# Performance work log

Measured on AMD Instinct MI355X. Metric: run time of the kernel, lower is better.

Reference implementation:

```python
import jax, jax.numpy as jnp
import numpy as np

NUM_HEADS = 16

def setup_inputs() -> dict:
    key = jax.random.key(0)
    k1, k2, k3 = jax.random.split(key, 3)
    B, N, C = 4, 4096, 1024
    x = jax.random.normal(k1, (B, N, C), dtype=jnp.float32)
    y = jax.random.normal(k2, (B, N, C), dtype=jnp.float32)
    # nn.Linear(embed_dim, embed_dim): weight [C, C], bias [C]
    W_proj = jax.random.normal(k3, (C, C), dtype=jnp.float32) * (1.0 / np.sqrt(C))
    b_proj = jnp.zeros((C,), dtype=jnp.float32)
    return {"x": x, "y": y, "W_proj": W_proj, "b_proj": b_proj}

def reference(x, y, W_proj, b_proj):
    B, N, C = x.shape
    H = NUM_HEADS
    d = C // H
    # NOTE: no head transpose in the original -> scores are over the HEAD axis.
    q = x.reshape(B, N, H, d)
    k = y.reshape(B, N, H, d)
    v = y.reshape(B, N, H, d)
    # attn: [B, N, H, H], per-token head-to-head scores
    attn = jnp.einsum('bnhd,bngd->bnhg', q, k) / jnp.sqrt(jnp.asarray(d, x.dtype))
    attn = jax.nn.softmax(attn, axis=-1)
    # dropout(p=0.1) is identity in eval mode
    o = jnp.einsum('bnhg,bngd->bnhd', attn, v)          # [B, N, H, d]
    # x.transpose(1, 2).reshape(B, N, C) in torch:
    o = jnp.transpose(o, (0, 2, 1, 3)).reshape(B, N, C)
    out = o @ W_proj.T + b_proj
    return out
```

## Files before the change

kernel.cpp:

```cpp
#include <hip/hip_runtime.h>
#include <hip/hip_bf16.h>
#include <stdint.h>

typedef __attribute__((ext_vector_type(8))) short bf16x8;
typedef __attribute__((ext_vector_type(4))) short bf16x4;
typedef __attribute__((ext_vector_type(4))) float f32x4;
typedef __attribute__((ext_vector_type(4))) int   i32x4;

static __device__ __forceinline__ short f2bs(float f) {
  __hip_bfloat16 h = __float2bfloat16(f);
  return __builtin_bit_cast(short, h);
}

__device__ __forceinline__ void gload_lds16(const void* g, void* l) {
  auto* gp = reinterpret_cast<__attribute__((address_space(1))) uint32_t*>((uintptr_t)g);
  auto* lp = reinterpret_cast<__attribute__((address_space(3))) uint32_t*>((uintptr_t)l);
  __builtin_amdgcn_global_load_lds(gp, lp, 16, 0, 0);
}

__global__ __launch_bounds__(256) void attn_kernel(
    const float* __restrict__ x, const float* __restrict__ y,
    __hip_bfloat16* __restrict__ A)
{
  const int wid  = threadIdx.x >> 6;
  const int lane = threadIdx.x & 63;
  const int tok  = blockIdx.x * 4 + wid;
  const int b    = tok >> 12;
  const int n    = tok & 4095;

  const float* xr = x + (size_t)tok * 1024;
  const float* yr = y + (size_t)tok * 1024;

  const int c  = lane & 15;
  const int qq = lane >> 4;

  const int fbase = c * 64 + qq * 8;
  bf16x8 yf[2], xf[2];
  #pragma unroll
  for (int kk = 0; kk < 2; ++kk) {
    const float4 a0 = *(const float4*)(yr + fbase + kk * 32);
    const float4 a1 = *(const float4*)(yr + fbase + kk * 32 + 4);
    const float4 b0 = *(const float4*)(xr + fbase + kk * 32);
    const float4 b1 = *(const float4*)(xr + fbase + kk * 32 + 4);
    yf[kk] = bf16x8{f2bs(a0.x), f2bs(a0.y), f2bs(a0.z), f2bs(a0.w),
                    f2bs(a1.x), f2bs(a1.y), f2bs(a1.z), f2bs(a1.w)};
    xf[kk] = bf16x8{f2bs(b0.x), f2bs(b0.y), f2bs(b0.z), f2bs(b0.w),
                    f2bs(b1.x), f2bs(b1.y), f2bs(b1.z), f2bs(b1.w)};
  }

  f32x4 acc = {0.f, 0.f, 0.f, 0.f};
  acc = __builtin_amdgcn_mfma_f32_16x16x32_bf16(yf[0], xf[0], acc, 0, 0, 0);
  acc = __builtin_amdgcn_mfma_f32_16x16x32_bf16(yf[1], xf[1], acc, 0, 0, 0);

  float sc[4];
  #pragma unroll
  for (int r = 0; r < 4; ++r) sc[r] = acc[r] * 0.125f;
  float mx = fmaxf(fmaxf(sc[0], sc[1]), fmaxf(sc[2], sc[3]));
  mx = fmaxf(mx, __shfl_xor(mx, 16));
  mx = fmaxf(mx, __shfl_xor(mx, 32));
  float e[4];
  #pragma unroll
  for (int r = 0; r < 4; ++r) e[r] = __expf(sc[r] - mx);
  float sm = (e[0] + e[1]) + (e[2] + e[3]);
  sm += __shfl_xor(sm, 16);
  sm += __shfl_xor(sm, 32);
  const float inv = 1.0f / sm;
  float p[4];
  #pragma unroll
  for (int r = 0; r < 4; ++r) p[r] = e[r] * inv;

  f32x4 o[4];
  #pragma unroll
  for (int q = 0; q < 4; ++q) o[q] = f32x4{0.f, 0.f, 0.f, 0.f};

#if __has_builtin(__builtin_amdgcn_mfma_f32_16x16x16bf16_1k)
  const bf16x4 pa = {f2bs(p[0]), f2bs(p[1]), f2bs(p[2]), f2bs(p[3])};
  #pragma unroll
  for (int q = 0; q < 4; ++q) {
    bf16x4 bq;
    #pragma unroll
    for (int j = 0; j < 4; ++j)
      bq[j] = f2bs(yr[(qq * 4 + j) * 64 + q * 16 + c]);
    o[q] = __builtin_amdgcn_mfma_f32_16x16x16bf16_1k(pa, bq, o[q], 0, 0, 0);
  }
#else
  const int u0 = ((int)(unsigned short)f2bs(p[1]) << 16) | (unsigned short)f2bs(p[0]);
  const int u1 = ((int)(unsigned short)f2bs(p[3]) << 16) | (unsigned short)f2bs(p[2]);
  const int s0 = c + 32 * qq;
  int a0 = __shfl(u0, s0), a1 = __shfl(u1, s0);
  int a2 = __shfl(u0, s0 + 16), a3 = __shfl(u1, s0 + 16);
  const bool valid = (qq < 2);
  if (!valid) { a0 = 0; a1 = 0; a2 = 0; a3 = 0; }
  const bf16x8 a8 = __builtin_bit_cast(bf16x8, i32x4{a0, a1, a2, a3});
  #pragma unroll
  for (int q = 0; q < 4; ++q) {
    bf16x8 b8;
    #pragma unroll
    for (int j = 0; j < 8; ++j) {
      const int g = (qq * 8 + j) & 15;
      const float v = yr[g * 64 + q * 16 + c];
      b8[j] = valid ? f2bs(v) : (short)0;
    }
    o[q] = __builtin_amdgcn_mfma_f32_16x16x32_bf16(a8, b8, o[q], 0, 0, 0);
  }
#endif

  const size_t base = ((size_t)b * 4096 + (n >> 4)) * 1024 + ((n & 15) << 6) + c;
  #pragma unroll
  for (int q = 0; q < 4; ++q)
    #pragma unroll
    for (int r = 0; r < 4; ++r) {
      const int h = qq * 4 + r;
      A[base + (size_t)h * 262144 + q * 16] = __float2bfloat16(o[q][r]);
    }
}

__global__ __launch_bounds__(256) void wcvt_kernel(const float* __restrict__ w,
                                                   __hip_bfloat16* __restrict__ wb)
{
  const int i = (blockIdx.x * 256 + threadIdx.x) * 4;
  const float4 v = *(const float4*)(w + i);
  wb[i + 0] = __float2bfloat16(v.x);
  wb[i + 1] = __float2bfloat16(v.y);
  wb[i + 2] = __float2bfloat16(v.z);
  wb[i + 3] = __float2bfloat16(v.w);
}

#define BM 128
#define BN 128
#define BK 32

__global__ __launch_bounds__(256) void gemm_bt_bias(
    const __hip_bfloat16* __restrict__ A,
    const __hip_bfloat16* __restrict__ Bw,
    const float* __restrict__ bias,
    float* __restrict__ C)
{
  constexpr int Nn = 1024, K = 1024;
  __shared__ __hip_bfloat16 As[BM * BK];
  __shared__ __hip_bfloat16 Bs[BN * BK];

  const int tid  = threadIdx.x;
  const int lane = tid & 63;
  const int wid  = tid >> 6;
  const int wr   = wid >> 1, wc = wid & 1;

  const int bid = blockIdx.y * 8 + blockIdx.x;
  const int nb  = (bid & 7) * 128 + (bid >> 3);
  const int mBase = (nb >> 3) * BM;
  const int nBase = (nb & 7) * BN;

  const int srow = tid >> 2;
  const int scol = (tid & 3) * 8;
  const __hip_bfloat16* aSrc0 = A  + (size_t)(mBase + srow)      * K + scol;
  const __hip_bfloat16* aSrc1 = A  + (size_t)(mBase + 64 + srow) * K + scol;
  const __hip_bfloat16* bSrc0 = Bw + (size_t)(nBase + srow)      * K + scol;
  const __hip_bfloat16* bSrc1 = Bw + (size_t)(nBase + 64 + srow) * K + scol;
  char* aDst0 = (char*)As + tid * 16;
  char* aDst1 = (char*)As + 4096 + tid * 16;
  char* bDst0 = (char*)Bs + tid * 16;
  char* bDst1 = (char*)Bs + 4096 + tid * 16;

  f32x4 acc[4][4];
  const f32x4 fzero = {0.f, 0.f, 0.f, 0.f};
  #pragma unroll
  for (int m = 0; m < 4; ++m)
    #pragma unroll
    for (int n = 0; n < 4; ++n) acc[m][n] = fzero;

  const int fr = lane & 15;
  const int kb = (lane >> 4) * 8;

  for (int k0 = 0; k0 < K; k0 += BK) {
    gload_lds16(aSrc0 + k0, aDst0);
    gload_lds16(aSrc1 + k0, aDst1);
    gload_lds16(bSrc0 + k0, bDst0);
    gload_lds16(bSrc1 + k0, bDst1);
    __syncthreads();

    bf16x8 af[4], bfr[4];
    #pragma unroll
    for (int m = 0; m < 4; ++m)
      af[m] = *(const bf16x8*)&As[(wr * 64 + m * 16 + fr) * BK + kb];
    #pragma unroll
    for (int n = 0; n < 4; ++n)
      bfr[n] = *(const bf16x8*)&Bs[(wc * 64 + n * 16 + fr) * BK + kb];

    #pragma unroll
    for (int m = 0; m < 4; ++m)
      #pragma unroll
      for (int n = 0; n < 4; ++n)
        acc[m][n] = __builtin_amdgcn_mfma_f32_16x16x32_bf16(af[m], bfr[n], acc[m][n], 0, 0, 0);
    __syncthreads();
  }

  const int fq = lane >> 4;
  #pragma unroll
  for (int n = 0; n < 4; ++n) {
    const int col = nBase + wc * 64 + n * 16 + fr;
    const float bv = bias[col];
    #pragma unroll
    for (int m = 0; m < 4; ++m) {
      const int row0 = mBase + wr * 64 + m * 16 + fq * 4;
      #pragma unroll
      for (int r = 0; r < 4; ++r)
        C[(size_t)(row0 + r) * Nn + col] = acc[m][n][r] + bv;
    }
  }
}

extern "C" void kernel_launch(void* const* d_in, const int* in_sizes, int n_in,
                              void* d_out, int out_size, void* d_ws, size_t ws_size,
                              hipStream_t stream) {
  const float* x    = (const float*)d_in[0];
  const float* y    = (const float*)d_in[1];
  const float* W    = (const float*)d_in[2];
  const float* bias = (const float*)d_in[3];
  float* out = (float*)d_out;

  __hip_bfloat16* Abuf = (__hip_bfloat16*)d_ws;
  __hip_bfloat16* Wbuf = (__hip_bfloat16*)((char*)d_ws + (size_t)16384 * 1024 * 2);

  wcvt_kernel<<<1024, 256, 0, stream>>>(W, Wbuf);
  attn_kernel<<<4096, 256, 0, stream>>>(x, y, Abuf);
  gemm_bt_bias<<<dim3(8, 128), 256, 0, stream>>>(Abuf, Wbuf, bias, out);
}
```

Baseline: 89.40 us.

## Replace projection GEMM with 256x256 double-buffered, swizzled 8-wave kernel

Rewrites the output projection GEMM to use 256x256 tiles with BK=64, 512 threads (8 waves), and double-buffered LDS. Global-to-LDS loads for the next K tile are issued while MFMAs run on the current one, and an XOR swizzle on LDS columns avoids bank conflicts. Explicit barriers, waitcnt and setprio interleave the load and compute phases. The aim is more data reuse per tile and hidden memory latency, at the cost of higher register/LDS use and only 256 blocks.

```diff
diff --git a/kernel.cpp b/kernel.cpp
--- a/kernel.cpp
+++ b/kernel.cpp
@@ -126,72 +126,143 @@
   wb[i + 3] = __float2bfloat16(v.w);
 }
 
-#define BM 128
-#define BN 128
-#define BK 32
-
-__global__ __launch_bounds__(256) void gemm_bt_bias(
+#define NT 16
+
+#define FENCE asm volatile("" ::: "memory")
+#define BAR   __builtin_amdgcn_s_barrier()
+
+#define STAGE_A(toff, b) do {                                           \
+    gload_lds16(aSrc + (toff),          aDst + (b) * 32768);            \
+    gload_lds16(aSrc + (toff) + 131072, aDst + (b) * 32768 + 8192);     \
+    gload_lds16(aSrc + (toff) + 262144, aDst + (b) * 32768 + 16384);    \
+    gload_lds16(aSrc + (toff) + 393216, aDst + (b) * 32768 + 24576);    \
+  } while (0)
+
+#define STAGE_B(toff, b) do {                                           \
+    gload_lds16(bSrc + (toff),          bDst + (b) * 32768);            \
+    gload_lds16(bSrc + (toff) + 131072, bDst + (b) * 32768 + 8192);     \
+    gload_lds16(bSrc + (toff) + 262144, bDst + (b) * 32768 + 16384);    \
+    gload_lds16(bSrc + (toff) + 393216, bDst + (b) * 32768 + 24576);    \
+  } while (0)
+
+__global__ __launch_bounds__(512, 2) void gemm256(
     const __hip_bfloat16* __restrict__ A,
     const __hip_bfloat16* __restrict__ Bw,
     const float* __restrict__ bias,
     float* __restrict__ C)
 {
-  constexpr int Nn = 1024, K = 1024;
-  __shared__ __hip_bfloat16 As[BM * BK];
-  __shared__ __hip_bfloat16 Bs[BN * BK];
+  constexpr int K = 1024, Nn = 1024;
+  __shared__ char ldsA[2 * 32768];
+  __shared__ char ldsB[2 * 32768];
 
   const int tid  = threadIdx.x;
   const int lane = tid & 63;
   const int wid  = tid >> 6;
-  const int wr   = wid >> 1, wc = wid & 1;
-
-  const int bid = blockIdx.y * 8 + blockIdx.x;
-  const int nb  = (bid & 7) * 128 + (bid >> 3);
-  const int mBase = (nb >> 3) * BM;
-  const int nBase = (nb & 7) * BN;
-
-  const int srow = tid >> 2;
-  const int scol = (tid & 3) * 8;
-  const __hip_bfloat16* aSrc0 = A  + (size_t)(mBase + srow)      * K + scol;
-  const __hip_bfloat16* aSrc1 = A  + (size_t)(mBase + 64 + srow) * K + scol;
-  const __hip_bfloat16* bSrc0 = Bw + (size_t)(nBase + srow)      * K + scol;
-  const __hip_bfloat16* bSrc1 = Bw + (size_t)(nBase + 64 + srow) * K + scol;
-  char* aDst0 = (char*)As + tid * 16;
-  char* aDst1 = (char*)As + 4096 + tid * 16;
-  char* bDst0 = (char*)Bs + tid * 16;
-  char* bDst1 = (char*)Bs + 4096 + tid * 16;
-
-  f32x4 acc[4][4];
-  const f32x4 fzero = {0.f, 0.f, 0.f, 0.f};
-  #pragma unroll
-  for (int m = 0; m < 4; ++m)
-    #pragma unroll
-    for (int n = 0; n < 4; ++n) acc[m][n] = fzero;
+  const int wr   = wid >> 2;
+  const int wc   = wid & 3;
+
+  const int bid = blockIdx.x;
+  const int nb  = (bid & 7) * 32 + (bid >> 3);
+  const int mBase = (nb >> 2) * 256;
+  const int nBase = (nb & 3) * 256;
+
+  const int srow = tid >> 3;
+  const int pcb  = (tid & 7) << 4;
+  const int lcb  = pcb ^ ((srow & 7) << 4);
+  const char* aSrc = (const char*)A  + ((size_t)(mBase + srow) * K) * 2 + lcb;
+  const char* bSrc = (const char*)Bw + ((size_t)(nBase + srow) * K) * 2 + lcb;
+  char* aDst = ldsA + tid * 16;
+  char* bDst = ldsB + tid * 16;
 
   const int fr = lane & 15;
-  const int kb = (lane >> 4) * 8;
-
-  for (int k0 = 0; k0 < K; k0 += BK) {
-    gload_lds16(aSrc0 + k0, aDst0);
-    gload_lds16(aSrc1 + k0, aDst1);
-    gload_lds16(bSrc0 + k0, bDst0);
-    gload_lds16(bSrc1 + k0, bDst1);
-    __syncthreads();
-
-    bf16x8 af[4], bfr[4];
-    #pragma unroll
-    for (int m = 0; m < 4; ++m)
-      af[m] = *(const bf16x8*)&As[(wr * 64 + m * 16 + fr) * BK + kb];
-    #pragma unroll
-    for (int n = 0; n < 4; ++n)
-      bfr[n] = *(const bf16x8*)&Bs[(wc * 64 + n * 16 + fr) * BK + kb];
-
-    #pragma unroll
-    for (int m = 0; m < 4; ++m)
-      #pragma unroll
-      for (int n = 0; n < 4; ++n)
-        acc[m][n] = __builtin_amdgcn_mfma_f32_16x16x32_bf16(af[m], bfr[n], acc[m][n], 0, 0, 0);
-    __syncthreads();
+  const int kq = lane >> 4;
+  const int xr = (fr & 7) << 4;
+  const int ofk0 = ((kq << 4))      ^ xr;
+  const int ofk1 = (64 + (kq << 4)) ^ xr;
+  const char* aRow = ldsA + (wr * 128 + fr) * 128;
+  const char* bRow = ldsB + (wc * 64  + fr) * 128;
+
+  f32x4 acc[8][4];
+  #pragma unroll
+  for (int m = 0; m < 8; ++m)
+    #pragma unroll
+    for (int n = 0; n < 4; ++n) acc[m][n] = f32x4{0.f, 0.f, 0.f, 0.f};
+
+  STAGE_A(0, 0);
+  STAGE_B(0, 0);
+  asm volatile("s_waitcnt vmcnt(0)" ::: "memory");
+  BAR;
+
+  for (int t = 0; t < NT; ++t) {
+    const int cur  = t & 1;
+    const int nxt  = cur ^ 1;
+    const int toff = (t + 1) * 128;
+    const char* aR = aRow + cur * 32768;
+    const char* bR = bRow + cur * 32768;
+    bf16x8 Af[4], Bf[4];
+
+    if (t + 1 < NT) STAGE_A(toff, nxt);
+    #pragma unroll
+    for (int n = 0; n < 4; ++n) Bf[n] = *(const bf16x8*)(bR + n * 2048 + ofk0);
+    #pragma unroll
+    for (int m = 0; m < 4; ++m) Af[m] = *(const bf16x8*)(aR + m * 2048 + ofk0);
+    FENCE; BAR;
+    asm volatile("s_waitcnt lgkmcnt(0)" ::: "memory");
+    __builtin_amdgcn_sched_barrier(0);
+    __builtin_amdgcn_s_setprio(1);
+    #pragma unroll
+    for (int m = 0; m < 4; ++m)
+      #pragma unroll
+      for (int n = 0; n < 4; ++n)
+        acc[m][n] = __builtin_amdgcn_mfma_f32_16x16x32_bf16(Af[m], Bf[n], acc[m][n], 0, 0, 0);
+    __builtin_amdgcn_s_setprio(0);
+    FENCE; BAR;
+
+    if (t + 1 < NT) STAGE_B(toff, nxt);
+    #pragma unroll
+    for (int m = 0; m < 4; ++m) Af[m] = *(const bf16x8*)(aR + (4 + m) * 2048 + ofk0);
+    FENCE; BAR;
+    asm volatile("s_waitcnt lgkmcnt(0)" ::: "memory");
+    __builtin_amdgcn_sched_barrier(0);
+    __builtin_amdgcn_s_setprio(1);
+    #pragma unroll
+    for (int m = 0; m < 4; ++m)
+      #pragma unroll
+      for (int n = 0; n < 4; ++n)
+        acc[4 + m][n] = __builtin_amdgcn_mfma_f32_16x16x32_bf16(Af[m], Bf[n], acc[4 + m][n], 0, 0, 0);
+    __builtin_amdgcn_s_setprio(0);
+    FENCE; BAR;
+
+    #pragma unroll
+    for (int n = 0; n < 4; ++n) Bf[n] = *(const bf16x8*)(bR + n * 2048 + ofk1);
+    #pragma unroll
+    for (int m = 0; m < 4; ++m) Af[m] = *(const bf16x8*)(aR + m * 2048 + ofk1);
+    FENCE; BAR;
+    asm volatile("s_waitcnt lgkmcnt(0)" ::: "memory");
+    __builtin_amdgcn_sched_barrier(0);
+    __builtin_amdgcn_s_setprio(1);
+    #pragma unroll
+    for (int m = 0; m < 4; ++m)
+      #pragma unroll
+      for (int n = 0; n < 4; ++n)
+        acc[m][n] = __builtin_amdgcn_mfma_f32_16x16x32_bf16(Af[m], Bf[n], acc[m][n], 0, 0, 0);
+    __builtin_amdgcn_s_setprio(0);
+    FENCE; BAR;
+
+    #pragma unroll
+    for (int m = 0; m < 4; ++m) Af[m] = *(const bf16x8*)(aR + (4 + m) * 2048 + ofk1);
+    FENCE; BAR;
+    asm volatile("s_waitcnt lgkmcnt(0)" ::: "memory");
+    __builtin_amdgcn_sched_barrier(0);
+    __builtin_amdgcn_s_setprio(1);
+    #pragma unroll
+    for (int m = 0; m < 4; ++m)
+      #pragma unroll
+      for (int n = 0; n < 4; ++n)
+        acc[4 + m][n] = __builtin_amdgcn_mfma_f32_16x16x32_bf16(Af[m], Bf[n], acc[4 + m][n], 0, 0, 0);
+    __builtin_amdgcn_s_setprio(0);
+    if (t + 1 < NT) asm volatile("s_waitcnt vmcnt(0)" ::: "memory");
+    FENCE; BAR;
   }
 
   const int fq = lane >> 4;
@@ -200,8 +271,8 @@
     const int col = nBase + wc * 64 + n * 16 + fr;
     const float bv = bias[col];
     #pragma unroll
-    for (int m = 0; m < 4; ++m) {
-      const int row0 = mBase + wr * 64 + m * 16 + fq * 4;
+    for (int m = 0; m < 8; ++m) {
+      const int row0 = mBase + wr * 128 + m * 16 + fq * 4;
       #pragma unroll
       for (int r = 0; r < 4; ++r)
         C[(size_t)(row0 + r) * Nn + col] = acc[m][n][r] + bv;
@@ -223,5 +294,5 @@
 
   wcvt_kernel<<<1024, 256, 0, stream>>>(W, Wbuf);
   attn_kernel<<<4096, 256, 0, stream>>>(x, y, Abuf);
-  gemm_bt_bias<<<dim3(8, 128), 256, 0, stream>>>(Abuf, Wbuf, bias, out);
-}
+  gemm256<<<256, 512, 0, stream>>>(Abuf, Wbuf, bias, out);
+}
```

New measurement: 76.39 us. -14.6%, faster.

## Triple-buffer GEMM LDS loads with XOR swizzle and manual waitcnt pipeline

Applied to the files above, without the earlier changes.

Rewrites the projection GEMM so it keeps three LDS stages in flight. Global-to-LDS loads for tile t+2 are issued while tile t is computed, with explicit vmcnt waits and a single barrier per tile, replacing the two syncthreads per K step. LDS addresses are XOR-swizzled to cut bank conflicts on the fragment reads. MFMA issue priority is raised and occupancy is hinted to 3 blocks per CU. This adds hand-written waitcnt ordering that must stay correct, and it uses more LDS per block.

```diff
diff --git a/kernel.cpp b/kernel.cpp
--- a/kernel.cpp
+++ b/kernel.cpp
@@ -126,78 +126,102 @@
   wb[i + 3] = __float2bfloat16(v.w);
 }
 
-#define BM 128
-#define BN 128
-#define BK 32
-
-__global__ __launch_bounds__(256) void gemm_bt_bias(
+#define NT 32
+
+#define FENCE asm volatile("" ::: "memory")
+#define BAR   __builtin_amdgcn_s_barrier()
+#define LGKM0 asm volatile("s_waitcnt lgkmcnt(0)" ::: "memory")
+#define VM4   asm volatile("s_waitcnt vmcnt(4)" ::: "memory")
+#define VM0   asm volatile("s_waitcnt vmcnt(0)" ::: "memory")
+#define SB0   __builtin_amdgcn_sched_barrier(0)
+#define SP1   __builtin_amdgcn_s_setprio(1)
+#define SP0   __builtin_amdgcn_s_setprio(0)
+
+#define STAGE(toff, bo) do {                                        \
+    gload_lds16(aSrc + (toff),          aDst + (bo));               \
+    gload_lds16(aSrc + (toff) + 131072, aDst + (bo) + 4096);        \
+    gload_lds16(bSrc + (toff),          bDst + (bo));               \
+    gload_lds16(bSrc + (toff) + 131072, bDst + (bo) + 4096);        \
+  } while (0)
+
+__global__ __launch_bounds__(256, 3) void gemm128(
     const __hip_bfloat16* __restrict__ A,
     const __hip_bfloat16* __restrict__ Bw,
     const float* __restrict__ bias,
     float* __restrict__ C)
 {
-  constexpr int Nn = 1024, K = 1024;
-  __shared__ __hip_bfloat16 As[BM * BK];
-  __shared__ __hip_bfloat16 Bs[BN * BK];
+  constexpr int K = 1024, Nn = 1024;
+  __shared__ char ldsA[3 * 8192];
+  __shared__ char ldsB[3 * 8192];
 
   const int tid  = threadIdx.x;
   const int lane = tid & 63;
   const int wid  = tid >> 6;
-  const int wr   = wid >> 1, wc = wid & 1;
-
-  const int bid = blockIdx.y * 8 + blockIdx.x;
+  const int wr   = wid >> 1;
+  const int wcN  = wid & 1;
+
+  const int bid = blockIdx.x;
   const int nb  = (bid & 7) * 128 + (bid >> 3);
-  const int mBase = (nb >> 3) * BM;
-  const int nBase = (nb & 7) * BN;
+  const int mBase = (nb >> 3) * 128;
+  const int nBase = (nb & 7) * 128;
 
   const int srow = tid >> 2;
-  const int scol = (tid & 3) * 8;
-  const __hip_bfloat16* aSrc0 = A  + (size_t)(mBase + srow)      * K + scol;
-  const __hip_bfloat16* aSrc1 = A  + (size_t)(mBase + 64 + srow) * K + scol;
-  const __hip_bfloat16* bSrc0 = Bw + (size_t)(nBase + srow)      * K + scol;
-  const __hip_bfloat16* bSrc1 = Bw + (size_t)(nBase + 64 + srow) * K + scol;
-  char* aDst0 = (char*)As + tid * 16;
-  char* aDst1 = (char*)As + 4096 + tid * 16;
-  char* bDst0 = (char*)Bs + tid * 16;
-  char* bDst1 = (char*)Bs + 4096 + tid * 16;
+  const int lcb  = (((tid & 3) ^ ((tid >> 3) & 3)) << 4);
+  const char* aSrc = (const char*)A  + (size_t)(mBase + srow) * (K * 2) + lcb;
+  const char* bSrc = (const char*)Bw + (size_t)(nBase + srow) * (K * 2) + lcb;
+  char* aDst = ldsA + tid * 16;
+  char* bDst = ldsB + tid * 16;
+
+  const int fr = lane & 15;
+  const int kq = lane >> 4;
+  const int ofk  = ((kq ^ ((fr >> 1) & 3)) << 4);
+  const int aOff = (wr  * 64 + fr) * 64 + ofk;
+  const int bOff = (wcN * 64 + fr) * 64 + ofk;
 
   f32x4 acc[4][4];
-  const f32x4 fzero = {0.f, 0.f, 0.f, 0.f};
   #pragma unroll
   for (int m = 0; m < 4; ++m)
     #pragma unroll
-    for (int n = 0; n < 4; ++n) acc[m][n] = fzero;
-
-  const int fr = lane & 15;
-  const int kb = (lane >> 4) * 8;
-
-  for (int k0 = 0; k0 < K; k0 += BK) {
-    gload_lds16(aSrc0 + k0, aDst0);
-    gload_lds16(aSrc1 + k0, aDst1);
-    gload_lds16(bSrc0 + k0, bDst0);
-    gload_lds16(bSrc1 + k0, bDst1);
-    __syncthreads();
-
-    bf16x8 af[4], bfr[4];
-    #pragma unroll
-    for (int m = 0; m < 4; ++m)
-      af[m] = *(const bf16x8*)&As[(wr * 64 + m * 16 + fr) * BK + kb];
-    #pragma unroll
-    for (int n = 0; n < 4; ++n)
-      bfr[n] = *(const bf16x8*)&Bs[(wc * 64 + n * 16 + fr) * BK + kb];
-
+    for (int n = 0; n < 4; ++n) acc[m][n] = f32x4{0.f, 0.f, 0.f, 0.f};
+
+  STAGE(0, 0);
+  STAGE(64, 8192);
+  VM4; FENCE; BAR; FENCE;
+
+  auto tile = [&](int t, int b0off, int b2off, int stg, int gate) {
+    if (stg) STAGE((t + 2) * 64, b2off);
+    bf16x8 Af[4], Bf[4];
+    const char* aB = ldsA + b0off + aOff;
+    const char* bB = ldsB + b0off + bOff;
+    #pragma unroll
+    for (int n = 0; n < 4; ++n) Bf[n] = *(const bf16x8*)(bB + n * 1024);
+    #pragma unroll
+    for (int m = 0; m < 4; ++m) Af[m] = *(const bf16x8*)(aB + m * 1024);
+    LGKM0; SB0;
+    SP1;
     #pragma unroll
     for (int m = 0; m < 4; ++m)
       #pragma unroll
       for (int n = 0; n < 4; ++n)
-        acc[m][n] = __builtin_amdgcn_mfma_f32_16x16x32_bf16(af[m], bfr[n], acc[m][n], 0, 0, 0);
-    __syncthreads();
-  }
+        acc[m][n] = __builtin_amdgcn_mfma_f32_16x16x32_bf16(Af[m], Bf[n], acc[m][n], 0, 0, 0);
+    SP0;
+    if (gate == 4) { VM4; }
+    else if (gate == 0) { VM0; }
+    FENCE; BAR; FENCE;
+  };
+
+  for (int t = 0; t < 30; t += 3) {
+    tile(t,     0,     16384, 1, 4);
+    tile(t + 1, 8192,  0,     1, 4);
+    tile(t + 2, 16384, 8192,  1, 4);
+  }
+  tile(30, 0,    0, 0, 0);
+  tile(31, 8192, 0, 0, -1);
 
   const int fq = lane >> 4;
   #pragma unroll
   for (int n = 0; n < 4; ++n) {
-    const int col = nBase + wc * 64 + n * 16 + fr;
+    const int col = nBase + wcN * 64 + n * 16 + fr;
     const float bv = bias[col];
     #pragma unroll
     for (int m = 0; m < 4; ++m) {
@@ -223,5 +247,5 @@
 
   wcvt_kernel<<<1024, 256, 0, stream>>>(W, Wbuf);
   attn_kernel<<<4096, 256, 0, stream>>>(x, y, Abuf);
-  gemm_bt_bias<<<dim3(8, 128), 256, 0, stream>>>(Abuf, Wbuf, bias, out);
-}
+  gemm128<<<1024, 256, 0, stream>>>(Abuf, Wbuf, bias, out);
+}
```

Measured after the change: 80.11 us. 10.4% less time.

## Keep a W panel resident in LDS and stream A from global; fuse W conversion

Applied to the files above, without the earlier changes.

Replaces the tiled LDS GEMM with a persistent-style kernel. Each 512-thread block loads a whole 64-column panel of bf16 W (128KB, XOR-swizzled) into LDS once, and each wave streams 128 rows of A directly from global into registers, double-buffered across k-steps. The fp32-to-bf16 conversion of W moves into the first 1024 blocks of the attention kernel, which removes one launch. The intent is to cut per-k-step barriers and repeated LDS staging of W. In exchange, A is re-read once per W panel, sixteen times in total, and the large LDS footprint limits occupancy to one block per CU, which makes global-load latency harder to hide.

```diff
diff --git a/kernel.cpp b/kernel.cpp
--- a/kernel.cpp
+++ b/kernel.cpp
@@ -20,8 +20,18 @@
 
 __global__ __launch_bounds__(256) void attn_kernel(
     const float* __restrict__ x, const float* __restrict__ y,
-    __hip_bfloat16* __restrict__ A)
+    __hip_bfloat16* __restrict__ A,
+    const float* __restrict__ W, __hip_bfloat16* __restrict__ Wb)
 {
+  if (blockIdx.x < 1024) {
+    const int i = (blockIdx.x * 256 + threadIdx.x) * 4;
+    const float4 v = *(const float4*)(W + i);
+    Wb[i + 0] = __float2bfloat16(v.x);
+    Wb[i + 1] = __float2bfloat16(v.y);
+    Wb[i + 2] = __float2bfloat16(v.z);
+    Wb[i + 3] = __float2bfloat16(v.w);
+  }
+
   const int wid  = threadIdx.x >> 6;
   const int lane = threadIdx.x & 63;
   const int tok  = blockIdx.x * 4 + wid;
@@ -115,96 +125,120 @@
     }
 }
 
-__global__ __launch_bounds__(256) void wcvt_kernel(const float* __restrict__ w,
-                                                   __hip_bfloat16* __restrict__ wb)
-{
-  const int i = (blockIdx.x * 256 + threadIdx.x) * 4;
-  const float4 v = *(const float4*)(w + i);
-  wb[i + 0] = __float2bfloat16(v.x);
-  wb[i + 1] = __float2bfloat16(v.y);
-  wb[i + 2] = __float2bfloat16(v.z);
-  wb[i + 3] = __float2bfloat16(v.w);
-}
-
-#define BM 128
-#define BN 128
-#define BK 32
-
-__global__ __launch_bounds__(256) void gemm_bt_bias(
+__global__ __launch_bounds__(512, 2) void gemm_stream(
     const __hip_bfloat16* __restrict__ A,
     const __hip_bfloat16* __restrict__ Bw,
     const float* __restrict__ bias,
     float* __restrict__ C)
 {
-  constexpr int Nn = 1024, K = 1024;
-  __shared__ __hip_bfloat16 As[BM * BK];
-  __shared__ __hip_bfloat16 Bs[BN * BK];
+  __shared__ char ldsW[131072];
 
   const int tid  = threadIdx.x;
   const int lane = tid & 63;
   const int wid  = tid >> 6;
-  const int wr   = wid >> 1, wc = wid & 1;
-
-  const int bid = blockIdx.y * 8 + blockIdx.x;
-  const int nb  = (bid & 7) * 128 + (bid >> 3);
-  const int mBase = (nb >> 3) * BM;
-  const int nBase = (nb & 7) * BN;
-
-  const int srow = tid >> 2;
-  const int scol = (tid & 3) * 8;
-  const __hip_bfloat16* aSrc0 = A  + (size_t)(mBase + srow)      * K + scol;
-  const __hip_bfloat16* aSrc1 = A  + (size_t)(mBase + 64 + srow) * K + scol;
-  const __hip_bfloat16* bSrc0 = Bw + (size_t)(nBase + srow)      * K + scol;
-  const __hip_bfloat16* bSrc1 = Bw + (size_t)(nBase + 64 + srow) * K + scol;
-  char* aDst0 = (char*)As + tid * 16;
-  char* aDst1 = (char*)As + 4096 + tid * 16;
-  char* bDst0 = (char*)Bs + tid * 16;
-  char* bDst1 = (char*)Bs + 4096 + tid * 16;
-
-  f32x4 acc[4][4];
-  const f32x4 fzero = {0.f, 0.f, 0.f, 0.f};
-  #pragma unroll
-  for (int m = 0; m < 4; ++m)
-    #pragma unroll
-    for (int n = 0; n < 4; ++n) acc[m][n] = fzero;
+
+  const int bid    = blockIdx.x;
+  const int mchunk = ((bid & 7) << 1) | ((bid >> 3) & 1);
+  const int npanel = bid >> 4;
+  const int nBase  = npanel * 64;
+  const int mWave  = mchunk * 1024 + wid * 128;
+
+  {
+    const int nrow = tid >> 7;
+    const int sl   = tid & 127;
+    #pragma unroll
+    for (int cc = 0; cc < 16; ++cc) {
+      const int row = cc * 4 + nrow;
+      gload_lds16((const char*)Bw + (size_t)(nBase + row) * 2048
+                                  + ((sl ^ (row & 7)) << 4),
+                  ldsW + cc * 8192 + tid * 16);
+    }
+    __syncthreads();
+  }
 
   const int fr = lane & 15;
-  const int kb = (lane >> 4) * 8;
-
-  for (int k0 = 0; k0 < K; k0 += BK) {
-    gload_lds16(aSrc0 + k0, aDst0);
-    gload_lds16(aSrc1 + k0, aDst1);
-    gload_lds16(bSrc0 + k0, bDst0);
-    gload_lds16(bSrc1 + k0, bDst1);
-    __syncthreads();
-
-    bf16x8 af[4], bfr[4];
-    #pragma unroll
-    for (int m = 0; m < 4; ++m)
-      af[m] = *(const bf16x8*)&As[(wr * 64 + m * 16 + fr) * BK + kb];
-    #pragma unroll
-    for (int n = 0; n < 4; ++n)
-      bfr[n] = *(const bf16x8*)&Bs[(wc * 64 + n * 16 + fr) * BK + kb];
-
+  const int kq = lane >> 4;
+
+  int bBase[4], bXs[4];
+  #pragma unroll
+  for (int nf = 0; nf < 4; ++nf) {
+    const int row = nf * 16 + fr;
+    const int h   = row & 7;
+    bBase[nf] = row * 2048 + ((kq ^ (h & 3)) << 4);
+    bXs[nf]   = (h >> 2);
+  }
+
+  const float* __restrict__ biasp = bias;
+
+  #pragma unroll 1
+  for (int s2 = 0; s2 < 2; ++s2) {
+    const int m0 = mWave + s2 * 64;
+    const char* aRow[4];
+    #pragma unroll
+    for (int mf = 0; mf < 4; ++mf)
+      aRow[mf] = (const char*)A + (size_t)(m0 + mf * 16 + fr) * 2048 + kq * 16;
+
+    f32x4 acc[4][4];
     #pragma unroll
     for (int m = 0; m < 4; ++m)
       #pragma unroll
-      for (int n = 0; n < 4; ++n)
-        acc[m][n] = __builtin_amdgcn_mfma_f32_16x16x32_bf16(af[m], bfr[n], acc[m][n], 0, 0, 0);
-    __syncthreads();
-  }
-
-  const int fq = lane >> 4;
-  #pragma unroll
-  for (int n = 0; n < 4; ++n) {
-    const int col = nBase + wc * 64 + n * 16 + fr;
-    const float bv = bias[col];
-    #pragma unroll
-    for (int m = 0; m < 4; ++m) {
-      const int row0 = mBase + wr * 64 + m * 16 + fq * 4;
+      for (int n = 0; n < 4; ++n) acc[m][n] = f32x4{0.f, 0.f, 0.f, 0.f};
+
+    bf16x8 A0[4], A1[4], B0[4], B1[4];
+
+    #pragma unroll
+    for (int mf = 0; mf < 4; ++mf) A0[mf] = *(const bf16x8*)(aRow[mf]);
+    #pragma unroll
+    for (int nf = 0; nf < 4; ++nf)
+      B0[nf] = *(const bf16x8*)(ldsW + bBase[nf] + (((0 ^ bXs[nf])) << 6));
+    #pragma unroll
+    for (int mf = 0; mf < 4; ++mf) A1[mf] = *(const bf16x8*)(aRow[mf] + 64);
+    #pragma unroll
+    for (int nf = 0; nf < 4; ++nf)
+      B1[nf] = *(const bf16x8*)(ldsW + bBase[nf] + (((1 ^ bXs[nf])) << 6));
+
+    for (int ks = 0; ks < 32; ks += 2) {
+      {
+        #pragma unroll
+        for (int m = 0; m < 4; ++m)
+          #pragma unroll
+          for (int n = 0; n < 4; ++n)
+            acc[m][n] = __builtin_amdgcn_mfma_f32_16x16x32_bf16(A0[m], B0[n], acc[m][n], 0, 0, 0);
+        const int kp = (ks + 2 < 32) ? (ks + 2) : 0;
+        #pragma unroll
+        for (int mf = 0; mf < 4; ++mf)
+          A0[mf] = *(const bf16x8*)(aRow[mf] + kp * 64);
+        #pragma unroll
+        for (int nf = 0; nf < 4; ++nf)
+          B0[nf] = *(const bf16x8*)(ldsW + bBase[nf] + ((kp ^ bXs[nf]) << 6));
+      }
+      {
+        #pragma unroll
+        for (int m = 0; m < 4; ++m)
+          #pragma unroll
+          for (int n = 0; n < 4; ++n)
+            acc[m][n] = __builtin_amdgcn_mfma_f32_16x16x32_bf16(A1[m], B1[n], acc[m][n], 0, 0, 0);
+        const int kp = (ks + 3 < 32) ? (ks + 3) : 1;
+        #pragma unroll
+        for (int mf = 0; mf < 4; ++mf)
+          A1[mf] = *(const bf16x8*)(aRow[mf] + kp * 64);
+        #pragma unroll
+        for (int nf = 0; nf < 4; ++nf)
+          B1[nf] = *(const bf16x8*)(ldsW + bBase[nf] + ((kp ^ bXs[nf]) << 6));
+      }
+    }
+
+    #pragma unroll
+    for (int n = 0; n < 4; ++n) {
+      const int col = nBase + n * 16 + fr;
+      const float bv = biasp[col];
       #pragma unroll
-      for (int r = 0; r < 4; ++r)
-        C[(size_t)(row0 + r) * Nn + col] = acc[m][n][r] + bv;
+      for (int m = 0; m < 4; ++m) {
+        const int row0 = m0 + m * 16 + kq * 4;
+        #pragma unroll
+        for (int r = 0; r < 4; ++r)
+          C[(size_t)(row0 + r) * 1024 + col] = acc[m][n][r] + bv;
+      }
     }
   }
 }
@@ -221,7 +255,6 @@
   __hip_bfloat16* Abuf = (__hip_bfloat16*)d_ws;
   __hip_bfloat16* Wbuf = (__hip_bfloat16*)((char*)d_ws + (size_t)16384 * 1024 * 2);
 
-  wcvt_kernel<<<1024, 256, 0, stream>>>(W, Wbuf);
-  attn_kernel<<<4096, 256, 0, stream>>>(x, y, Abuf);
-  gemm_bt_bias<<<dim3(8, 128), 256, 0, stream>>>(Abuf, Wbuf, bias, out);
-}
+  attn_kernel<<<4096, 256, 0, stream>>>(x, y, Abuf, W, Wbuf);
+  gemm_stream<<<256, 512, 0, stream>>>(Abuf, Wbuf, bias, out);
+}
```

Result: slower. 103.9 us (+16.2%).
